# Performance work log

Hardware: AMD Instinct MI355X
Metric: run time of the kernel (lower is better)

## Reference

```python
import jax, jax.numpy as jnp
import numpy as np

RATIO = 0.9375  # config.ratio


def setup_inputs() -> dict:
    key = jax.random.key(0)
    x = jax.random.normal(key, (4096, 8192), dtype=jnp.float32)
    return {"x": x}


def reference(x):
    # recall_window(x, ratio, dim=-1, keepdim=False)
    # For each row: sort, then find the minimum-length window covering
    # target = int(ratio * N) consecutive sorted values; return (left, right).
    N = x.shape[-1]
    target = int(RATIO * N)
    s = jnp.sort(x, axis=-1)                       # [R, N]
    # window_length[i] = s[i + target - 1] - s[i], for i in [0, N - target]
    lengths = s[:, target - 1:] - s[:, : N - target + 1]   # [R, N - target + 1]
    idx = jnp.argmin(lengths, axis=-1)             # first min, matches '<' in loop
    left = jnp.take_along_axis(s, idx[:, None], axis=-1)[:, 0]
    right = jnp.take_along_axis(s, (idx + target - 1)[:, None], axis=-1)[:, 0]
    return left, right
```

## Files before the change

### kernel.cpp

```cpp
#include <hip/hip_runtime.h>
#include <stdint.h>

#define ROWS   4096
#define NCOL   8192
#define TARGET 7680
#define NW     (NCOL - TARGET + 1)
#define NT     256
#define VPT    (NCOL / NT)
#define NB     2048
#define NSB    1024
#define SCAP   3072
#define MAXS   (SCAP / NT)

struct Smem {
    uint32_t hist[NB];
    float    sorted[SCAP];
    uint32_t wsum[8];
    uint32_t res[4];
    uint32_t aux[2];
    float    fmin[4], fmax[4];
    float    rv[4];
    int      ri[4];
};

__device__ __forceinline__ int bin1f(float v, float mn, float s) {
    int b = (int)((v - mn) * s);
    return b < 0 ? 0 : (b > NB - 1 ? NB - 1 : b);
}
__device__ __forceinline__ int sbin_bot(float v, float mn, float sb) {
    int b = (int)((v - mn) * sb);
    return b < 0 ? 0 : (b > NSB - 1 ? NSB - 1 : b);
}
__device__ __forceinline__ int sbin_top(float v, float mx, float st) {
    int b = (int)((mx - v) * st);
    b = b < 0 ? 0 : (b > NSB - 1 ? NSB - 1 : b);
    return (NSB - 1) - b;
}

__device__ void locate2(Smem& sm, uint32_t ka, uint32_t kb, int tid) {
    const int lane = tid & 63, wid = tid >> 6;
    const int base = tid * 8;
    uint32_t h[8], s0 = 0;
    #pragma unroll
    for (int j = 0; j < 8; j++) { h[j] = sm.hist[base + j]; s0 += h[j]; }
    uint32_t sc = s0;
    #pragma unroll
    for (int off = 1; off < 64; off <<= 1) {
        uint32_t n = __shfl_up(sc, off, 64);
        if (lane >= off) sc += n;
    }
    if (lane == 63) sm.wsum[wid] = sc;
    __syncthreads();
    uint32_t woff = 0;
    for (int w = 0; w < wid; w++) woff += sm.wsum[w];
    uint32_t incl = sc + woff, excl = incl - s0;
    if (ka >= excl && ka < incl) {
        uint32_t c = excl; bool done = false;
        #pragma unroll
        for (int j = 0; j < 8; j++) {
            if (!done) {
                if (ka < c + h[j]) { sm.res[0] = (uint32_t)(base + j); done = true; }
                else c += h[j];
            }
        }
    }
    if (kb >= excl && kb < incl) {
        uint32_t c = excl; bool done = false;
        #pragma unroll
        for (int j = 0; j < 8; j++) {
            if (!done) {
                if (kb < c + h[j]) { sm.res[2] = (uint32_t)(base + j); done = true; }
                else c += h[j];
            }
        }
    }
    __syncthreads();
}

__device__ void scan_offsets(Smem& sm, int tid) {
    const int lane = tid & 63, wid = tid >> 6;
    const int base = tid * 8;
    uint32_t h[8], s0 = 0;
    #pragma unroll
    for (int j = 0; j < 8; j++) { h[j] = sm.hist[base + j]; s0 += h[j]; }
    uint32_t sc = s0;
    #pragma unroll
    for (int off = 1; off < 64; off <<= 1) {
        uint32_t n = __shfl_up(sc, off, 64);
        if (lane >= off) sc += n;
    }
    if (lane == 63) sm.wsum[wid] = sc;
    __syncthreads();
    uint32_t woff = 0;
    for (int w = 0; w < wid; w++) woff += sm.wsum[w];
    uint32_t run = sc - s0 + woff;
    if (tid == (NSB / 8)) sm.aux[0] = run;
    #pragma unroll
    for (int j = 0; j < 8; j++) { sm.hist[base + j] = run; run += h[j]; }
    if (tid == NT - 1) sm.aux[1] = run;
    __syncthreads();
}

__global__ __launch_bounds__(NT, 4)
void recall_window_kernel(const float* __restrict__ x, float* __restrict__ out) {
    __shared__ Smem sm;
    const int tid = threadIdx.x;
    const int row = blockIdx.x;
    const int lane = tid & 63, wid = tid >> 6;

    float v[VPT];
    const float4* xv = (const float4*)(x + (size_t)row * NCOL);
    #pragma unroll
    for (int j = 0; j < VPT / 4; j++) {
        float4 t = xv[tid + j * NT];
        v[4 * j + 0] = t.x; v[4 * j + 1] = t.y;
        v[4 * j + 2] = t.z; v[4 * j + 3] = t.w;
    }

    float mn = v[0], mx = v[0];
    #pragma unroll
    for (int j = 1; j < VPT; j++) { mn = fminf(mn, v[j]); mx = fmaxf(mx, v[j]); }
    #pragma unroll
    for (int off = 32; off > 0; off >>= 1) {
        mn = fminf(mn, __shfl_down(mn, off, 64));
        mx = fmaxf(mx, __shfl_down(mx, off, 64));
    }
    if (lane == 0) { sm.fmin[wid] = mn; sm.fmax[wid] = mx; }
    #pragma unroll
    for (int j = 0; j < 8; j++) sm.hist[tid + j * NT] = 0;
    __syncthreads();
    mn = fminf(fminf(sm.fmin[0], sm.fmin[1]), fminf(sm.fmin[2], sm.fmin[3]));
    mx = fmaxf(fmaxf(sm.fmax[0], sm.fmax[1]), fmaxf(sm.fmax[2], sm.fmax[3]));

    if (!(mx > mn)) {
        if (tid == 0) { out[row] = mn; out[ROWS + row] = mn; }
        return;
    }
    const float scale1 = (float)NB / (mx - mn);

    #pragma unroll
    for (int j = 0; j < VPT; j++) atomicAdd(&sm.hist[bin1f(v[j], mn, scale1)], 1u);
    __syncthreads();
    locate2(sm, NW - 1, TARGET - 1, tid);
    const int B_lo = (int)sm.res[0];
    const int B_hi = (int)sm.res[2];

    #pragma unroll
    for (int j = 0; j < 8; j++) sm.hist[tid + j * NT] = 0;
    __syncthreads();
    const float scale_b = (float)NSB * scale1 / (float)(B_lo + 1);
    const float scale_t = (float)NSB * scale1 / (float)(NB - B_hi);
    #pragma unroll
    for (int j = 0; j < VPT; j++) {
        float val = v[j];
        int b1 = bin1f(val, mn, scale1);
        if (b1 <= B_lo)      atomicAdd(&sm.hist[sbin_bot(val, mn, scale_b)], 1u);
        else if (b1 >= B_hi) atomicAdd(&sm.hist[NSB + sbin_top(val, mx, scale_t)], 1u);
    }
    __syncthreads();
    scan_offsets(sm, tid);
    const uint32_t cb  = sm.aux[0];
    uint32_t tot = sm.aux[1]; if (tot > SCAP) tot = SCAP;

    #pragma unroll
    for (int j = 0; j < VPT; j++) {
        float val = v[j];
        int b1 = bin1f(val, mn, scale1);
        int gb = -1;
        if (b1 <= B_lo)      gb = sbin_bot(val, mn, scale_b);
        else if (b1 >= B_hi) gb = NSB + sbin_top(val, mx, scale_t);
        if (gb >= 0) {
            uint32_t pos = atomicAdd(&sm.hist[gb], 1u);
            if (pos < SCAP) sm.sorted[pos] = val;
        }
    }
    __syncthreads();

    int   tgt[MAXS];
    float fvv[MAXS];
    #pragma unroll
    for (int it = 0; it < MAXS; it++) {
        int s = tid + it * NT;
        tgt[it] = -1;
        if (s < (int)tot) {
            float vv = sm.sorted[s];
            int gb = (s < (int)cb) ? sbin_bot(vv, mn, scale_b)
                                   : (NSB + sbin_top(vv, mx, scale_t));
            uint32_t start = (gb == 0) ? 0u : sm.hist[gb - 1];
            uint32_t end   = sm.hist[gb];
            if (end > SCAP) end = SCAP;
            uint32_t r = 0;
            if (end - start > 1) {
                for (uint32_t q = start; q < end; q++) {
                    float u = sm.sorted[q];
                    r += (u < vv) || (u == vv && (int)q < s);
                }
            }
            tgt[it] = (int)(start + r);
            fvv[it] = vv;
        }
    }
    __syncthreads();
    #pragma unroll
    for (int it = 0; it < MAXS; it++)
        if (tgt[it] >= 0) sm.sorted[tgt[it]] = fvv[it];
    __syncthreads();


    const int topstart = (int)tot - NW;
    float lbest = __int_as_float(0x7F800000);
    int   lidx  = 0x7FFFFFFF;
    for (int i = tid; i < NW; i += NT) {
        float len = sm.sorted[topstart + i] - sm.sorted[i];
        if (len < lbest) { lbest = len; lidx = i; }
    }
    #pragma unroll
    for (int off = 32; off > 0; off >>= 1) {
        float v2 = __shfl_down(lbest, off, 64);
        int   i2 = __shfl_down(lidx,  off, 64);
        if (v2 < lbest || (v2 == lbest && i2 < lidx)) { lbest = v2; lidx = i2; }
    }
    if (lane == 0) { sm.rv[wid] = lbest; sm.ri[wid] = lidx; }
    __syncthreads();
    if (tid == 0) {
        float bv = sm.rv[0]; int bi = sm.ri[0];
        #pragma unroll
        for (int w = 1; w < 4; w++) {
            float v2 = sm.rv[w]; int i2 = sm.ri[w];
            if (v2 < bv || (v2 == bv && i2 < bi)) { bv = v2; bi = i2; }
        }
        out[row]        = sm.sorted[bi];
        out[ROWS + row] = sm.sorted[topstart + bi];
    }
}

extern "C" void kernel_launch(void* const* d_in, const int* in_sizes, int n_in,
                              void* d_out, int out_size, void* d_ws, size_t ws_size,
                              hipStream_t stream) {
    const float* x = (const float*)d_in[0];
    float* out = (float*)d_out;
    recall_window_kernel<<<ROWS, NT, 0, stream>>>(x, out);
}
```

Baseline: 224.1 us.

## Scatter tail elements using first-level histogram bins, dropping second histogram pass

Measured after the change: 196.4 us. 1.14x faster.

```diff
diff --git a/kernel.cpp b/kernel.cpp
--- a/kernel.cpp
+++ b/kernel.cpp
@@ -8,16 +8,15 @@
 #define NT     256
 #define VPT    (NCOL / NT)
 #define NB     2048
-#define NSB    1024
-#define SCAP   3072
+#define SCAP   2048
 #define MAXS   (SCAP / NT)
 
 struct Smem {
     uint32_t hist[NB];
     float    sorted[SCAP];
-    uint32_t wsum[8];
+    float    sorted2[SCAP];
+    uint32_t wsum[4];
     uint32_t res[4];
-    uint32_t aux[2];
     float    fmin[4], fmax[4];
     float    rv[4];
     int      ri[4];
@@ -27,79 +26,7 @@
     int b = (int)((v - mn) * s);
     return b < 0 ? 0 : (b > NB - 1 ? NB - 1 : b);
 }
-__device__ __forceinline__ int sbin_bot(float v, float mn, float sb) {
-    int b = (int)((v - mn) * sb);
-    return b < 0 ? 0 : (b > NSB - 1 ? NSB - 1 : b);
-}
-__device__ __forceinline__ int sbin_top(float v, float mx, float st) {
-    int b = (int)((mx - v) * st);
-    b = b < 0 ? 0 : (b > NSB - 1 ? NSB - 1 : b);
-    return (NSB - 1) - b;
-}
-
-__device__ void locate2(Smem& sm, uint32_t ka, uint32_t kb, int tid) {
-    const int lane = tid & 63, wid = tid >> 6;
-    const int base = tid * 8;
-    uint32_t h[8], s0 = 0;
-    #pragma unroll
-    for (int j = 0; j < 8; j++) { h[j] = sm.hist[base + j]; s0 += h[j]; }
-    uint32_t sc = s0;
-    #pragma unroll
-    for (int off = 1; off < 64; off <<= 1) {
-        uint32_t n = __shfl_up(sc, off, 64);
-        if (lane >= off) sc += n;
-    }
-    if (lane == 63) sm.wsum[wid] = sc;
-    __syncthreads();
-    uint32_t woff = 0;
-    for (int w = 0; w < wid; w++) woff += sm.wsum[w];
-    uint32_t incl = sc + woff, excl = incl - s0;
-    if (ka >= excl && ka < incl) {
-        uint32_t c = excl; bool done = false;
-        #pragma unroll
-        for (int j = 0; j < 8; j++) {
-            if (!done) {
-                if (ka < c + h[j]) { sm.res[0] = (uint32_t)(base + j); done = true; }
-                else c += h[j];
-            }
-        }
-    }
-    if (kb >= excl && kb < incl) {
-        uint32_t c = excl; bool done = false;
-        #pragma unroll
-        for (int j = 0; j < 8; j++) {
-            if (!done) {
-                if (kb < c + h[j]) { sm.res[2] = (uint32_t)(base + j); done = true; }
-                else c += h[j];
-            }
-        }
-    }
-    __syncthreads();
-}
-
-__device__ void scan_offsets(Smem& sm, int tid) {
-    const int lane = tid & 63, wid = tid >> 6;
-    const int base = tid * 8;
-    uint32_t h[8], s0 = 0;
-    #pragma unroll
-    for (int j = 0; j < 8; j++) { h[j] = sm.hist[base + j]; s0 += h[j]; }
-    uint32_t sc = s0;
-    #pragma unroll
-    for (int off = 1; off < 64; off <<= 1) {
-        uint32_t n = __shfl_up(sc, off, 64);
-        if (lane >= off) sc += n;
-    }
-    if (lane == 63) sm.wsum[wid] = sc;
-    __syncthreads();
-    uint32_t woff = 0;
-    for (int w = 0; w < wid; w++) woff += sm.wsum[w];
-    uint32_t run = sc - s0 + woff;
-    if (tid == (NSB / 8)) sm.aux[0] = run;
-    #pragma unroll
-    for (int j = 0; j < 8; j++) { sm.hist[base + j] = run; run += h[j]; }
-    if (tid == NT - 1) sm.aux[1] = run;
-    __syncthreads();
-}
+__device__ __forceinline__ int HIX(int b) { return ((b & 7) << 8) | (b >> 3); }
 
 __global__ __launch_bounds__(NT, 4)
 void recall_window_kernel(const float* __restrict__ x, float* __restrict__ out) {
@@ -139,71 +66,103 @@
     const float scale1 = (float)NB / (mx - mn);
 
     #pragma unroll
-    for (int j = 0; j < VPT; j++) atomicAdd(&sm.hist[bin1f(v[j], mn, scale1)], 1u);
-    __syncthreads();
-    locate2(sm, NW - 1, TARGET - 1, tid);
-    const int B_lo = (int)sm.res[0];
-    const int B_hi = (int)sm.res[2];
-
-    #pragma unroll
-    for (int j = 0; j < 8; j++) sm.hist[tid + j * NT] = 0;
-    __syncthreads();
-    const float scale_b = (float)NSB * scale1 / (float)(B_lo + 1);
-    const float scale_t = (float)NSB * scale1 / (float)(NB - B_hi);
+    for (int j = 0; j < VPT; j++)
+        atomicAdd(&sm.hist[HIX(bin1f(v[j], mn, scale1))], 1u);
+    __syncthreads();
+
+    uint32_t h[8], s0 = 0;
+    #pragma unroll
+    for (int j = 0; j < 8; j++) { h[j] = sm.hist[(j << 8) | tid]; s0 += h[j]; }
+    uint32_t sc = s0;
+    #pragma unroll
+    for (int off = 1; off < 64; off <<= 1) {
+        uint32_t n = __shfl_up(sc, off, 64);
+        if (lane >= off) sc += n;
+    }
+    if (lane == 63) sm.wsum[wid] = sc;
+    __syncthreads();
+    uint32_t woff = 0;
+    for (int w = 0; w < wid; w++) woff += sm.wsum[w];
+    const uint32_t incl = sc + woff, excl = incl - s0;
+    const uint32_t ka = NW - 1, kb = TARGET - 1;
+    if (ka >= excl && ka < incl) {
+        uint32_t c = excl; bool done = false;
+        #pragma unroll
+        for (int j = 0; j < 8; j++) {
+            if (!done) {
+                if (ka < c + h[j]) {
+                    sm.res[0] = (uint32_t)(tid * 8 + j);
+                    sm.res[1] = c + h[j];
+                    done = true;
+                } else c += h[j];
+            }
+        }
+    }
+    if (kb >= excl && kb < incl) {
+        uint32_t c = excl; bool done = false;
+        #pragma unroll
+        for (int j = 0; j < 8; j++) {
+            if (!done) {
+                if (kb < c + h[j]) {
+                    sm.res[2] = (uint32_t)(tid * 8 + j);
+                    sm.res[3] = c;
+                    done = true;
+                } else c += h[j];
+            }
+        }
+    }
+    {
+        uint32_t run = excl;
+        #pragma unroll
+        for (int j = 0; j < 8; j++) { sm.hist[(j << 8) | tid] = run; run += h[j]; }
+    }
+    __syncthreads();
+    const int      B_lo    = (int)sm.res[0];
+    const uint32_t cntB    = sm.res[1];
+    const int      B_hi    = (int)sm.res[2];
+    const uint32_t topBase = sm.res[3];
+    const uint32_t shiftT  = cntB - topBase;
+    uint32_t tot = cntB + (uint32_t)NCOL - topBase;
+    if (tot > SCAP) tot = SCAP;
+
     #pragma unroll
     for (int j = 0; j < VPT; j++) {
         float val = v[j];
-        int b1 = bin1f(val, mn, scale1);
-        if (b1 <= B_lo)      atomicAdd(&sm.hist[sbin_bot(val, mn, scale_b)], 1u);
-        else if (b1 >= B_hi) atomicAdd(&sm.hist[NSB + sbin_top(val, mx, scale_t)], 1u);
-    }
-    __syncthreads();
-    scan_offsets(sm, tid);
-    const uint32_t cb  = sm.aux[0];
-    uint32_t tot = sm.aux[1]; if (tot > SCAP) tot = SCAP;
-
-    #pragma unroll
-    for (int j = 0; j < VPT; j++) {
-        float val = v[j];
-        int b1 = bin1f(val, mn, scale1);
-        int gb = -1;
-        if (b1 <= B_lo)      gb = sbin_bot(val, mn, scale_b);
-        else if (b1 >= B_hi) gb = NSB + sbin_top(val, mx, scale_t);
-        if (gb >= 0) {
-            uint32_t pos = atomicAdd(&sm.hist[gb], 1u);
+        int b = bin1f(val, mn, scale1);
+        if (b <= B_lo || b >= B_hi) {
+            uint32_t pos = atomicAdd(&sm.hist[HIX(b)], 1u);
+            if (b >= B_hi) pos += shiftT;
             if (pos < SCAP) sm.sorted[pos] = val;
         }
     }
     __syncthreads();
 
-    int   tgt[MAXS];
-    float fvv[MAXS];
     #pragma unroll
     for (int it = 0; it < MAXS; it++) {
         int s = tid + it * NT;
-        tgt[it] = -1;
         if (s < (int)tot) {
             float vv = sm.sorted[s];
-            int gb = (s < (int)cb) ? sbin_bot(vv, mn, scale_b)
-                                   : (NSB + sbin_top(vv, mx, scale_t));
-            uint32_t start = (gb == 0) ? 0u : sm.hist[gb - 1];
-            uint32_t end   = sm.hist[gb];
-            if (end > SCAP) end = SCAP;
+            int b = bin1f(vv, mn, scale1);
+            uint32_t en = sm.hist[HIX(b)];
+            uint32_t st;
+            if (s < (int)cntB) {
+                st = (b == 0) ? 0u : sm.hist[HIX(b - 1)];
+            } else {
+                st = (b == B_hi) ? topBase : sm.hist[HIX(b - 1)];
+                st += shiftT; en += shiftT;
+            }
+            if (en > tot) en = tot;
             uint32_t r = 0;
-            if (end - start > 1) {
-                for (uint32_t q = start; q < end; q++) {
+            if (en - st > 1) {
+                for (uint32_t q = st; q < en; q++) {
                     float u = sm.sorted[q];
                     r += (u < vv) || (u == vv && (int)q < s);
                 }
             }
-            tgt[it] = (int)(start + r);
-            fvv[it] = vv;
-        }
-    }
-    __syncthreads();
-    #pragma unroll
-    for (int it = 0; it < MAXS; it++)
-        if (tgt[it] >= 0) sm.sorted[tgt[it]] = fvv[it];
+            uint32_t d = st + r;
+            if (d < SCAP) sm.sorted2[d] = vv;
+        }
+    }
     __syncthreads();
 
 
@@ -211,7 +170,7 @@
     float lbest = __int_as_float(0x7F800000);
     int   lidx  = 0x7FFFFFFF;
     for (int i = tid; i < NW; i += NT) {
-        float len = sm.sorted[topstart + i] - sm.sorted[i];
+        float len = sm.sorted2[topstart + i] - sm.sorted2[i];
         if (len < lbest) { lbest = len; lidx = i; }
     }
     #pragma unroll
@@ -229,8 +188,8 @@
             float v2 = sm.rv[w]; int i2 = sm.ri[w];
             if (v2 < bv || (v2 == bv && i2 < bi)) { bv = v2; bi = i2; }
         }
-        out[row]        = sm.sorted[bi];
-        out[ROWS + row] = sm.sorted[topstart + bi];
+        out[row]        = sm.sorted2[bi];
+        out[ROWS + row] = sm.sorted2[topstart + bi];
     }
 }
 
```
